# Optimization experiments

Measured on AMD Instinct MI355X. Metric: run time of the kernel, lower is better.

## Reference

```python
import jax, jax.numpy as jnp
import numpy as np

BETA = 0.9
NORM_EPS = 1e-12  # torch F.normalize default eps


def _sqdist(u, v):
    # ||u||^2 + ||v||^2 - 2 u v^T  (matches module's dist())
    return (u ** 2).sum(1, keepdims=True) + (v ** 2).sum(1) - 2.0 * u @ v.T


def setup_inputs() -> dict:
    key = jax.random.key(0)
    k1, k2 = jax.random.split(key)
    z = jax.random.normal(k1, (16, 4096, 128), dtype=jnp.float32)
    # codebook: unit-norm rows (Hypersphere.random_uniform init)
    w = jax.random.normal(k2, (1024, 128), dtype=jnp.float32)
    emb_w = w / jnp.linalg.norm(w, axis=1, keepdims=True)
    return {"z": z, "emb_w": emb_w}


def reference(z, emb_w):
    B, N, D = z.shape
    n_e = emb_w.shape[0]
    zf = z.reshape(-1, D)  # [B*N, D]

    # codebook self-distances + stats
    cd = _sqdist(emb_w, emb_w)                      # [n_e, n_e]
    min_distance = jnp.sort(cd, axis=0)[1]          # kthvalue(cd, 2, dim=0)
    mean_cb_distance = min_distance.mean()
    mean_cb_variance = jnp.var(cd, axis=1, ddof=1).mean()  # torch.var unbiased

    # quantisation: argmin over codebook
    d = _sqdist(zf, emb_w)                          # [B*N, n_e]
    idx = jnp.argmin(d, axis=1)                     # [B*N]
    z_q = emb_w[idx].reshape(z.shape)               # [B, N, D]

    # F.normalize default dim=1 applied to the 3D tensor -> normalize over N axis
    zn = z_q / jnp.maximum(jnp.linalg.norm(z_q, axis=1, keepdims=True), NORM_EPS)

    sg = jax.lax.stop_gradient
    # legacy loss
    loss = jnp.mean((sg(z_q) - z) ** 2) + BETA * jnp.mean((z_q - sg(z)) ** 2)

    # straight-through estimator
    z_q_st = z + sg(z_q - z)

    # sampled_idx buffer of length B*n_e, scatter 1s at the encoding indices
    sampled_idx = jnp.zeros(B * n_e, dtype=z.dtype).at[idx].set(1.0).reshape(B, n_e)

    si = idx.reshape(B, N)
    return (z_q_st, loss, sampled_idx, idx.reshape(B, -1),
            mean_cb_variance, mean_cb_distance, si, zn)
```

## Files before the change

kernel.cpp:

```cpp
#include <hip/hip_runtime.h>
#include <math.h>

#define D       128
#define NE      1024
#define NROWS   65536
#define NB      16

#define OUT_ZQ    0
#define OUT_LOSS  8388608
#define OUT_SAMP  8388609
#define OUT_IDX   8404993
#define OUT_VAR   8470529
#define OUT_DIST  8470530
#define OUT_SI    8470531
#define OUT_ZN    8536067

#define SCR       8536068
#define SCR_WL    (SCR + 65536)
#define SCR_CNT   (SCR + 131072)
#define SCR_LIST  (SCR + 131073)

#define WS_IDX    0
#define WS_WW     65536
#define WS_FLAGS  66560
#define WS_MIN2   67584
#define WS_VAR    68608
#define WS_LOSSP  69632
#define WS_COLSQP 70144
#define WS_COLSQ  135680

#define MARGIN 2e-3f

typedef __attribute__((ext_vector_type(8))) short s16x8;
typedef __attribute__((ext_vector_type(4))) float f32x4;

#define GLDS16(gp, lp)                                                        \
  __builtin_amdgcn_global_load_lds(                                           \
      (const __attribute__((address_space(1))) unsigned int*)(gp),            \
      (__attribute__((address_space(3))) unsigned int*)(lp), 16, 0, 0)

__device__ __forceinline__ unsigned short f2bf(float f) {
  unsigned int u = __float_as_uint(f);
  return (unsigned short)((u + 0x7FFFu + ((u >> 16) & 1u)) >> 16);
}
__device__ __forceinline__ float bf2f(unsigned short h) {
  return __uint_as_float(((unsigned int)h) << 16);
}

__device__ __forceinline__ float npsq_sum128(const float* p) {
  float a[8];
#pragma unroll
  for (int m = 0; m < 8; ++m) a[m] = __fmul_rn(p[m], p[m]);
  for (int k = 8; k < 128; k += 8) {
#pragma unroll
    for (int m = 0; m < 8; ++m) a[m] = __fadd_rn(a[m], __fmul_rn(p[k + m], p[k + m]));
  }
  float s01 = __fadd_rn(a[0], a[1]);
  float s23 = __fadd_rn(a[2], a[3]);
  float s45 = __fadd_rn(a[4], a[5]);
  float s67 = __fadd_rn(a[6], a[7]);
  return __fadd_rn(__fadd_rn(s01, s23), __fadd_rn(s45, s67));
}

__global__ __launch_bounds__(256) void k_wsplit(const float* __restrict__ w,
                                                float* __restrict__ out,
                                                float* __restrict__ ws) {
  int u = blockIdx.x * 256 + threadIdx.x;
  int c = u >> 4, j = u & 15;
  const float4* p = (const float4*)(w + c * D + j * 8);
  float4 f0 = p[0], f1 = p[1];
  float ff[8] = {f0.x, f0.y, f0.z, f0.w, f1.x, f1.y, f1.z, f1.w};
  s16x8 h, l;
#pragma unroll
  for (int e = 0; e < 8; ++e) {
    unsigned short hb = f2bf(ff[e]);
    h[e] = (short)hb;
    l[e] = (short)f2bf(ff[e] - bf2f(hb));
  }
  unsigned int by = ((unsigned int)(c * 256 + j * 16)) ^ ((unsigned int)((c & 15) << 4));
  *(s16x8*)((char*)(out + SCR) + by)    = h;
  *(s16x8*)((char*)(out + SCR_WL) + by) = l;
  if (u < NE) {
    ws[WS_WW + u] = npsq_sum128(w + u * D);
    ((int*)ws)[WS_FLAGS + u] = 0;
  }
  if (u == 0) ((int*)out)[SCR_CNT] = 0;
}

__global__ __launch_bounds__(256) void k_cb(const float* __restrict__ w,
                                            float* __restrict__ wsf,
                                            float* __restrict__ out) {
  __shared__ unsigned short Lw[2][16384];
  __shared__ float Lww[1024];
  const int t    = threadIdx.x;
  const int lane = t & 63;
  const int wq   = t >> 6;
  const int n    = lane & 15;
  const int q    = lane >> 4;
  const int i0   = blockIdx.x * 64 + wq * 16;

  const unsigned short* whg = (const unsigned short*)(out + SCR);
  const unsigned short* wlg = (const unsigned short*)(out + SCR_WL);

#define CSTAGE(BUF, P) do {                                              \
    const unsigned short* _wh = whg + (size_t)(P) * 8192;                \
    const unsigned short* _wl = wlg + (size_t)(P) * 8192;                \
    _Pragma("unroll")                                                    \
    for (int _it = 0; _it < 4; ++_it) {                                  \
      int _ci = _it * 256 + t;                                           \
      GLDS16(_wh + _ci * 8, &Lw[BUF][_ci * 8]);                          \
      GLDS16(_wl + _ci * 8, &Lw[BUF][8192 + _ci * 8]);                   \
    } } while (0)

  CSTAGE(0, 0);
  for (int i = t; i < 1024; i += 256) Lww[i] = wsf[WS_WW + i];

  s16x8 AH[4], AL[4];
  {
    const float* wr = w + (size_t)(i0 + n) * D;
#pragma unroll
    for (int ks = 0; ks < 4; ++ks) {
      float4 f0 = *(const float4*)(wr + ks * 32 + q * 8);
      float4 f1 = *(const float4*)(wr + ks * 32 + q * 8 + 4);
      float ff[8] = {f0.x, f0.y, f0.z, f0.w, f1.x, f1.y, f1.z, f1.w};
      s16x8 h, l;
#pragma unroll
      for (int j = 0; j < 8; ++j) {
        unsigned short hb = f2bf(ff[j]);
        h[j] = (short)hb;
        l[j] = (short)f2bf(ff[j] - bf2f(hb));
      }
      AH[ks] = h; AL[ks] = l;
    }
  }
  float wwi[4];
#pragma unroll
  for (int r = 0; r < 4; ++r) wwi[r] = wsf[WS_WW + i0 + q * 4 + r];

  float m1[4], m2[4], S[4], Q[4];
#pragma unroll
  for (int r = 0; r < 4; ++r) { m1[r] = INFINITY; m2[r] = INFINITY; S[r] = 0.f; Q[r] = 0.f; }

  __syncthreads();

  for (int p = 0; p < 16; ++p) {
    const int buf = p & 1;
    if (p < 15) CSTAGE(buf ^ 1, p + 1);

    for (int ct = 0; ct < 4; ++ct) {
      const int cL = ct * 16 + n;
      const int c  = p * 64 + cL;
      const float wwj = Lww[c];
      f32x4 aX = (f32x4){0.f, 0.f, 0.f, 0.f};
      f32x4 aY = (f32x4){0.f, 0.f, 0.f, 0.f};
#pragma unroll
      for (int ks = 0; ks < 4; ++ks) {
        unsigned int off = (unsigned int)(cL * 256) +
                           (((unsigned int)(64 * ks + 16 * q)) ^ ((unsigned int)(cL & 15) << 4));
        s16x8 BH = *(const s16x8*)((const char*)&Lw[buf][0] + off);
        s16x8 BL = *(const s16x8*)((const char*)&Lw[buf][8192] + off);
        aX = __builtin_amdgcn_mfma_f32_16x16x32_bf16(AH[ks], BH, aX, 0, 0, 0);
        aY = __builtin_amdgcn_mfma_f32_16x16x32_bf16(AH[ks], BL, aY, 0, 0, 0);
        aY = __builtin_amdgcn_mfma_f32_16x16x32_bf16(AL[ks], BH, aY, 0, 0, 0);
      }
#pragma unroll
      for (int r = 0; r < 4; ++r) {
        float dot = aX[r] + aY[r];
        float d = __fsub_rn(__fadd_rn(wwi[r], wwj), __fmul_rn(2.f, dot));
        if (d < m1[r]) { m2[r] = m1[r]; m1[r] = d; } else m2[r] = fminf(m2[r], d);
        S[r] += d; Q[r] = fmaf(d, d, Q[r]);
      }
    }
    __syncthreads();
  }

#pragma unroll
  for (int r = 0; r < 4; ++r) {
    float a1 = m1[r], a2 = m2[r], s = S[r], qq = Q[r];
#pragma unroll
    for (int mask = 1; mask < 16; mask <<= 1) {
      float b1 = __shfl_xor(a1, mask, 64);
      float b2 = __shfl_xor(a2, mask, 64);
      float bs = __shfl_xor(s,  mask, 64);
      float bq = __shfl_xor(qq, mask, 64);
      a2 = fminf(fminf(a2, b2), fmaxf(a1, b1));
      a1 = fminf(a1, b1);
      s += bs; qq += bq;
    }
    if (n == 0) {
      int row = i0 + q * 4 + r;
      wsf[WS_MIN2 + row] = a2;
      wsf[WS_VAR + row] = (qq - s * s / (float)NE) / (float)(NE - 1);
    }
  }
#undef CSTAGE
}

__global__ __launch_bounds__(512, 2) void k_qmfma(const float* __restrict__ z,
                                                  float* __restrict__ wsf,
                                                  float* __restrict__ out) {
  __shared__ unsigned short Lw[2][16384];
  __shared__ float Lww[1024];
  const int t    = threadIdx.x;
  const int lane = t & 63;
  const int wq   = t >> 6;
  const int n    = lane & 15;
  const int q    = lane >> 4;
  const int rowb = blockIdx.x * 256 + wq * 32;

  const unsigned short* whg = (const unsigned short*)(out + SCR);
  const unsigned short* wlg = (const unsigned short*)(out + SCR_WL);

#define QSTAGE(BUF, P) do {                                              \
    const unsigned short* _wh = whg + (size_t)(P) * 8192;                \
    const unsigned short* _wl = wlg + (size_t)(P) * 8192;                \
    _Pragma("unroll")                                                    \
    for (int _it = 0; _it < 2; ++_it) {                                  \
      int _ci = _it * 512 + t;                                           \
      GLDS16(_wh + _ci * 8, &Lw[BUF][_ci * 8]);                          \
      GLDS16(_wl + _ci * 8, &Lw[BUF][8192 + _ci * 8]);                   \
    } } while (0)

  QSTAGE(0, 0);
  for (int i = t; i < 1024; i += 512) Lww[i] = wsf[WS_WW + i];

  s16x8 AH[2][4], AL[2][4];
#pragma unroll
  for (int rt = 0; rt < 2; ++rt) {
    const float* zr = z + (size_t)(rowb + rt * 16 + n) * D;
#pragma unroll
    for (int ks = 0; ks < 4; ++ks) {
      float4 f0 = *(const float4*)(zr + ks * 32 + q * 8);
      float4 f1 = *(const float4*)(zr + ks * 32 + q * 8 + 4);
      float ff[8] = {f0.x, f0.y, f0.z, f0.w, f1.x, f1.y, f1.z, f1.w};
      s16x8 h, l;
#pragma unroll
      for (int j = 0; j < 8; ++j) {
        unsigned short hb = f2bf(ff[j]);
        h[j] = (short)hb;
        l[j] = (short)f2bf(ff[j] - bf2f(hb));
      }
      AH[rt][ks] = h; AL[rt][ks] = l;
    }
  }

  float m1[2][4], m2[2][4]; int i1[2][4];
#pragma unroll
  for (int rt = 0; rt < 2; ++rt)
#pragma unroll
    for (int r = 0; r < 4; ++r) { m1[rt][r] = INFINITY; m2[rt][r] = INFINITY; i1[rt][r] = 0; }

  __syncthreads();

  for (int p = 0; p < 16; ++p) {
    const int buf = p & 1;
    if (p < 15) QSTAGE(buf ^ 1, p + 1);

    for (int ct = 0; ct < 4; ++ct) {
      const int cL = ct * 16 + n;
      const int c  = p * 64 + cL;
      const float wwc = Lww[c];
      f32x4 aX[2], aY[2];
#pragma unroll
      for (int rt = 0; rt < 2; ++rt) {
        aX[rt] = (f32x4){0.f, 0.f, 0.f, 0.f};
        aY[rt] = (f32x4){0.f, 0.f, 0.f, 0.f};
      }
#pragma unroll
      for (int ks = 0; ks < 4; ++ks) {
        unsigned int off = (unsigned int)(cL * 256) +
                           (((unsigned int)(64 * ks + 16 * q)) ^ ((unsigned int)(cL & 15) << 4));
        s16x8 BH = *(const s16x8*)((const char*)&Lw[buf][0] + off);
        s16x8 BL = *(const s16x8*)((const char*)&Lw[buf][8192] + off);
#pragma unroll
        for (int rt = 0; rt < 2; ++rt) {
          aX[rt] = __builtin_amdgcn_mfma_f32_16x16x32_bf16(AH[rt][ks], BH, aX[rt], 0, 0, 0);
          aY[rt] = __builtin_amdgcn_mfma_f32_16x16x32_bf16(AH[rt][ks], BL, aY[rt], 0, 0, 0);
          aY[rt] = __builtin_amdgcn_mfma_f32_16x16x32_bf16(AL[rt][ks], BH, aY[rt], 0, 0, 0);
        }
      }
#pragma unroll
      for (int rt = 0; rt < 2; ++rt)
#pragma unroll
        for (int r = 0; r < 4; ++r) {
          float v = fmaf(-2.f, aX[rt][r] + aY[rt][r], wwc);
          if (v < m1[rt][r]) { m2[rt][r] = m1[rt][r]; m1[rt][r] = v; i1[rt][r] = c; }
          else m2[rt][r] = fminf(m2[rt][r], v);
        }
    }
    __syncthreads();
  }

#pragma unroll
  for (int rt = 0; rt < 2; ++rt)
#pragma unroll
    for (int r = 0; r < 4; ++r) {
      float a1 = m1[rt][r], a2 = m2[rt][r]; int ai = i1[rt][r];
#pragma unroll
      for (int mask = 1; mask < 16; mask <<= 1) {
        float b1 = __shfl_xor(a1, mask, 64);
        float b2 = __shfl_xor(a2, mask, 64);
        int   bi = __shfl_xor(ai, mask, 64);
        a2 = fminf(fminf(a2, b2), fmaxf(a1, b1));
        bool take = (b1 < a1) || (b1 == a1 && bi < ai);
        a1 = take ? b1 : a1; ai = take ? bi : ai;
      }
      if (n == 0) {
        int grow = rowb + rt * 16 + q * 4 + r;
        if (a2 - a1 > MARGIN) {
          ((int*)wsf)[WS_IDX + grow] = ai;
          out[OUT_IDX + grow] = (float)ai;
          out[OUT_SI  + grow] = (float)ai;
          ((int*)wsf)[WS_FLAGS + ai] = 1;
        } else {
          int pos = atomicAdd(((int*)out) + SCR_CNT, 1);
          ((int*)out)[SCR_LIST + pos] = grow;
        }
      }
    }
#undef QSTAGE
}

__global__ __launch_bounds__(256) void k_fallback(const float* __restrict__ z,
                                                  const float* __restrict__ w,
                                                  float* __restrict__ wsf,
                                                  float* __restrict__ out) {
  const int t = threadIdx.x;
  const int count = ((const int*)out)[SCR_CNT];
  const int* list = ((const int*)out) + SCR_LIST;
  __shared__ float zrow[128];
  __shared__ float zzs;
  __shared__ float rv[256];
  __shared__ int   ri[256];
  for (int i = blockIdx.x; i < count; i += gridDim.x) {
    int row = list[i];
    __syncthreads();
    if (t < 32) ((float4*)zrow)[t] = ((const float4*)(z + (size_t)row * D))[t];
    __syncthreads();
    if (t < 8) {
      float a = __fmul_rn(zrow[t], zrow[t]);
#pragma unroll
      for (int k = 8; k < 128; k += 8)
        a = __fadd_rn(a, __fmul_rn(zrow[k + t], zrow[k + t]));
      float s1 = __fadd_rn(a,  __shfl_xor(a, 1, 64));
      float s2 = __fadd_rn(s1, __shfl_xor(s1, 2, 64));
      float s3 = __fadd_rn(s2, __shfl_xor(s2, 4, 64));
      if (t == 0) zzs = s3;
    }
    __syncthreads();
    float zz = zzs;
    float bv = INFINITY; int bi = 0;
    const float4* z4 = (const float4*)zrow;
    for (int cc = 0; cc < 4; ++cc) {
      int c = cc * 256 + t;
      const float4* wp = (const float4*)(w + (size_t)c * D);
      float acc = 0.f;
#pragma unroll
      for (int k4 = 0; k4 < 32; ++k4) {
        float4 a = wp[k4];
        float4 zv = z4[k4];
        acc = fmaf(zv.x, a.x, acc); acc = fmaf(zv.y, a.y, acc);
        acc = fmaf(zv.z, a.z, acc); acc = fmaf(zv.w, a.w, acc);
      }
      float d = __fsub_rn(__fadd_rn(zz, wsf[WS_WW + c]), __fmul_rn(2.f, acc));
      if (d < bv) { bv = d; bi = c; }
    }
    rv[t] = bv; ri[t] = bi;
    __syncthreads();
    for (int s = 128; s > 0; s >>= 1) {
      if (t < s) {
        float v2 = rv[t + s]; int i2 = ri[t + s];
        if (v2 < rv[t] || (v2 == rv[t] && i2 < ri[t])) { rv[t] = v2; ri[t] = i2; }
      }
      __syncthreads();
    }
    if (t == 0) {
      int mi = ri[0];
      ((int*)wsf)[WS_IDX + row] = mi;
      out[OUT_IDX + row] = (float)mi;
      out[OUT_SI  + row] = (float)mi;
      ((int*)wsf)[WS_FLAGS + mi] = 1;
    }
  }
}

__global__ __launch_bounds__(256) void k_gather(const float* __restrict__ z,
                                                const float* __restrict__ w,
                                                float* __restrict__ ws,
                                                float* __restrict__ out) {
  __shared__ float csp[32][8][4];
  __shared__ float lred[256];
  const int t = threadIdx.x, blk = blockIdx.x;
  const int c4 = t & 31, rg = t >> 5;
  float lp = 0.f;
  float csx = 0.f, csy = 0.f, csz = 0.f, csw = 0.f;
  for (int m = 0; m < 16; ++m) {
    int r  = rg + 8 * m;
    int gr = blk * 128 + r;
    int idx = ((const int*)ws)[WS_IDX + gr];
    float4 qv = *(const float4*)&w[idx * D + c4 * 4];
    float4 zv = *(const float4*)&z[(size_t)gr * D + c4 * 4];
    *(float4*)&out[OUT_ZQ + (size_t)gr * D + c4 * 4] = qv;
    float dx = qv.x - zv.x, dy = qv.y - zv.y, dz = qv.z - zv.z, dw = qv.w - zv.w;
    lp = fmaf(dx, dx, lp); lp = fmaf(dy, dy, lp);
    lp = fmaf(dz, dz, lp); lp = fmaf(dw, dw, lp);
    csx = fmaf(qv.x, qv.x, csx); csy = fmaf(qv.y, qv.y, csy);
    csz = fmaf(qv.z, qv.z, csz); csw = fmaf(qv.w, qv.w, csw);
  }
  csp[c4][rg][0] = csx; csp[c4][rg][1] = csy;
  csp[c4][rg][2] = csz; csp[c4][rg][3] = csw;
  lred[t] = lp;
  __syncthreads();
  for (int s = 128; s > 0; s >>= 1) {
    if (t < s) lred[t] += lred[t + s];
    __syncthreads();
  }
  if (t == 0) ws[WS_LOSSP + blk] = lred[0];
  if (t < 128) {
    int dcol = t;
    float s = 0.f;
    for (int g = 0; g < 8; ++g) s += csp[dcol >> 2][g][dcol & 3];
    ws[WS_COLSQP + blk * 128 + dcol] = s;
  }
}

__global__ __launch_bounds__(256) void k_zn(const float* __restrict__ ws,
                                            const float* __restrict__ w,
                                            float* __restrict__ out) {
  const int t = threadIdx.x, blk = blockIdx.x;
  const int c4 = t & 31, rg = t >> 5;
  const int b = blk >> 5;
  float csx = 0.f, csy = 0.f, csz = 0.f, csw = 0.f;
  for (int rb = 0; rb < 32; ++rb) {
    float4 pp = *(const float4*)&ws[WS_COLSQP + (size_t)(b * 32 + rb) * 128 + c4 * 4];
    csx += pp.x; csy += pp.y; csz += pp.z; csw += pp.w;
  }
  float nx = fmaxf(sqrtf(csx), 1e-12f);
  float ny = fmaxf(sqrtf(csy), 1e-12f);
  float nz = fmaxf(sqrtf(csz), 1e-12f);
  float nw = fmaxf(sqrtf(csw), 1e-12f);
  for (int m = 0; m < 16; ++m) {
    int gr = blk * 128 + rg + 8 * m;
    int idx = ((const int*)ws)[WS_IDX + gr];
    float4 qv = *(const float4*)&w[idx * D + c4 * 4];
    size_t o = (size_t)gr * D + c4 * 4;
    out[OUT_ZN + o + 0] = qv.x / nx;
    out[OUT_ZN + o + 1] = qv.y / ny;
    out[OUT_ZN + o + 2] = qv.z / nz;
    out[OUT_ZN + o + 3] = qv.w / nw;
  }
  if (blk == 0) {
    __shared__ float f1[256], f2[256], f3[256];
    __syncthreads();
    f1[t] = ws[WS_LOSSP + t] + ws[WS_LOSSP + t + 256];
    f2[t] = (ws[WS_MIN2 + t] + ws[WS_MIN2 + t + 512]) +
            (ws[WS_MIN2 + t + 256] + ws[WS_MIN2 + t + 768]);
    f3[t] = (ws[WS_VAR + t] + ws[WS_VAR + t + 512]) +
            (ws[WS_VAR + t + 256] + ws[WS_VAR + t + 768]);
    __syncthreads();
    for (int s = 128; s > 0; s >>= 1) {
      if (t < s) { f1[t] += f1[t + s]; f2[t] += f2[t + s]; f3[t] += f3[t + s]; }
      __syncthreads();
    }
    if (t == 0) {
      float m = f1[0] / 8388608.f;
      out[OUT_LOSS] = m + 0.9f * m;
      out[OUT_VAR]  = f3[0] / 1024.f;
      out[OUT_DIST] = f2[0] / 1024.f;
    }
    const int* flags = (const int*)ws + WS_FLAGS;
    for (int i = t; i < NB * NE; i += 256)
      out[OUT_SAMP + i] = (i < NE && flags[i] != 0) ? 1.f : 0.f;
  }
}

extern "C" void kernel_launch(void* const* d_in, const int* in_sizes, int n_in,
                              void* d_out, int out_size, void* d_ws, size_t ws_size,
                              hipStream_t stream) {
  const float* z = (const float*)d_in[0];
  const float* w = (const float*)d_in[1];
  float* out = (float*)d_out;
  float* ws  = (float*)d_ws;

  hipLaunchKernelGGL(k_wsplit,   dim3(64),   dim3(256), 0, stream, w, out, ws);
  hipLaunchKernelGGL(k_cb,       dim3(16),   dim3(256), 0, stream, w, ws, out);
  hipLaunchKernelGGL(k_qmfma,    dim3(256),  dim3(512), 0, stream, z, ws, out);
  hipLaunchKernelGGL(k_fallback, dim3(1024), dim3(256), 0, stream, z, w, ws, out);
  hipLaunchKernelGGL(k_gather,   dim3(512),  dim3(256), 0, stream, z, w, ws, out);
  hipLaunchKernelGGL(k_zn,       dim3(512),  dim3(256), 0, stream, ws, w, out);
}
```

Before: 134.7 us.

## Split codebook self-distance kernel across more blocks with per-wave column ranges

The codebook statistics kernel now runs 64 blocks, each handling 16 codebook rows. Each of its four waves covers a quarter of the columns, reading the bf16 split codebook straight from global memory instead of double-buffering it through LDS. Per-wave min/second-min/sum/sum-of-squares partials are merged through shared memory at the end. This aims to raise parallelism in a small 16-block kernel that sits serially before the main quantisation kernel, at the cost of more redundant global/L2 reads of the codebook and an extra cross-wave reduction.

```diff
diff --git a/kernel.cpp b/kernel.cpp
--- a/kernel.cpp
+++ b/kernel.cpp
@@ -90,30 +90,16 @@
 __global__ __launch_bounds__(256) void k_cb(const float* __restrict__ w,
                                             float* __restrict__ wsf,
                                             float* __restrict__ out) {
-  __shared__ unsigned short Lw[2][16384];
-  __shared__ float Lww[1024];
+  __shared__ float cm1[4][16], cm2[4][16], cS[4][16], cQ[4][16];
   const int t    = threadIdx.x;
   const int lane = t & 63;
   const int wq   = t >> 6;
   const int n    = lane & 15;
   const int q    = lane >> 4;
-  const int i0   = blockIdx.x * 64 + wq * 16;
-
-  const unsigned short* whg = (const unsigned short*)(out + SCR);
-  const unsigned short* wlg = (const unsigned short*)(out + SCR_WL);
-
-#define CSTAGE(BUF, P) do {                                              \
-    const unsigned short* _wh = whg + (size_t)(P) * 8192;                \
-    const unsigned short* _wl = wlg + (size_t)(P) * 8192;                \
-    _Pragma("unroll")                                                    \
-    for (int _it = 0; _it < 4; ++_it) {                                  \
-      int _ci = _it * 256 + t;                                           \
-      GLDS16(_wh + _ci * 8, &Lw[BUF][_ci * 8]);                          \
-      GLDS16(_wl + _ci * 8, &Lw[BUF][8192 + _ci * 8]);                   \
-    } } while (0)
-
-  CSTAGE(0, 0);
-  for (int i = t; i < 1024; i += 256) Lww[i] = wsf[WS_WW + i];
+  const int i0   = blockIdx.x * 16;
+
+  const char* whg = (const char*)(out + SCR);
+  const char* wlg = (const char*)(out + SCR_WL);
 
   s16x8 AH[4], AL[4];
   {
@@ -141,37 +127,28 @@
 #pragma unroll
   for (int r = 0; r < 4; ++r) { m1[r] = INFINITY; m2[r] = INFINITY; S[r] = 0.f; Q[r] = 0.f; }
 
-  __syncthreads();
-
-  for (int p = 0; p < 16; ++p) {
-    const int buf = p & 1;
-    if (p < 15) CSTAGE(buf ^ 1, p + 1);
-
-    for (int ct = 0; ct < 4; ++ct) {
-      const int cL = ct * 16 + n;
-      const int c  = p * 64 + cL;
-      const float wwj = Lww[c];
-      f32x4 aX = (f32x4){0.f, 0.f, 0.f, 0.f};
-      f32x4 aY = (f32x4){0.f, 0.f, 0.f, 0.f};
-#pragma unroll
-      for (int ks = 0; ks < 4; ++ks) {
-        unsigned int off = (unsigned int)(cL * 256) +
-                           (((unsigned int)(64 * ks + 16 * q)) ^ ((unsigned int)(cL & 15) << 4));
-        s16x8 BH = *(const s16x8*)((const char*)&Lw[buf][0] + off);
-        s16x8 BL = *(const s16x8*)((const char*)&Lw[buf][8192] + off);
-        aX = __builtin_amdgcn_mfma_f32_16x16x32_bf16(AH[ks], BH, aX, 0, 0, 0);
-        aY = __builtin_amdgcn_mfma_f32_16x16x32_bf16(AH[ks], BL, aY, 0, 0, 0);
-        aY = __builtin_amdgcn_mfma_f32_16x16x32_bf16(AL[ks], BH, aY, 0, 0, 0);
-      }
-#pragma unroll
-      for (int r = 0; r < 4; ++r) {
-        float dot = aX[r] + aY[r];
-        float d = __fsub_rn(__fadd_rn(wwi[r], wwj), __fmul_rn(2.f, dot));
-        if (d < m1[r]) { m2[r] = m1[r]; m1[r] = d; } else m2[r] = fminf(m2[r], d);
-        S[r] += d; Q[r] = fmaf(d, d, Q[r]);
-      }
-    }
-    __syncthreads();
+  for (int ct = 0; ct < 16; ++ct) {
+    const int c = wq * 256 + ct * 16 + n;
+    const float wwj = wsf[WS_WW + c];
+    f32x4 aX = (f32x4){0.f, 0.f, 0.f, 0.f};
+    f32x4 aY = (f32x4){0.f, 0.f, 0.f, 0.f};
+#pragma unroll
+    for (int ks = 0; ks < 4; ++ks) {
+      unsigned int off = (unsigned int)(c * 256) +
+                         (((unsigned int)(64 * ks + 16 * q)) ^ ((unsigned int)((c & 15) << 4)));
+      s16x8 BH = *(const s16x8*)(whg + off);
+      s16x8 BL = *(const s16x8*)(wlg + off);
+      aX = __builtin_amdgcn_mfma_f32_16x16x32_bf16(AH[ks], BH, aX, 0, 0, 0);
+      aY = __builtin_amdgcn_mfma_f32_16x16x32_bf16(AH[ks], BL, aY, 0, 0, 0);
+      aY = __builtin_amdgcn_mfma_f32_16x16x32_bf16(AL[ks], BH, aY, 0, 0, 0);
+    }
+#pragma unroll
+    for (int r = 0; r < 4; ++r) {
+      float dot = aX[r] + aY[r];
+      float d = __fsub_rn(__fadd_rn(wwi[r], wwj), __fmul_rn(2.f, dot));
+      if (d < m1[r]) { m2[r] = m1[r]; m1[r] = d; } else m2[r] = fminf(m2[r], d);
+      S[r] += d; Q[r] = fmaf(d, d, Q[r]);
+    }
   }
 
 #pragma unroll
@@ -188,12 +165,23 @@
       s += bs; qq += bq;
     }
     if (n == 0) {
-      int row = i0 + q * 4 + r;
-      wsf[WS_MIN2 + row] = a2;
-      wsf[WS_VAR + row] = (qq - s * s / (float)NE) / (float)(NE - 1);
-    }
-  }
-#undef CSTAGE
+      int rl = q * 4 + r;
+      cm1[wq][rl] = a1; cm2[wq][rl] = a2; cS[wq][rl] = s; cQ[wq][rl] = qq;
+    }
+  }
+  __syncthreads();
+  if (t < 16) {
+    float a1 = cm1[0][t], a2 = cm2[0][t], s = cS[0][t], qq = cQ[0][t];
+#pragma unroll
+    for (int v = 1; v < 4; ++v) {
+      float b1 = cm1[v][t], b2 = cm2[v][t];
+      a2 = fminf(fminf(a2, b2), fmaxf(a1, b1));
+      a1 = fminf(a1, b1);
+      s += cS[v][t]; qq += cQ[v][t];
+    }
+    wsf[WS_MIN2 + i0 + t] = a2;
+    wsf[WS_VAR + i0 + t] = (qq - s * s / (float)NE) / (float)(NE - 1);
+  }
 }
 
 __global__ __launch_bounds__(512, 2) void k_qmfma(const float* __restrict__ z,
@@ -483,7 +471,7 @@
   float* ws  = (float*)d_ws;
 
   hipLaunchKernelGGL(k_wsplit,   dim3(64),   dim3(256), 0, stream, w, out, ws);
-  hipLaunchKernelGGL(k_cb,       dim3(16),   dim3(256), 0, stream, w, ws, out);
+  hipLaunchKernelGGL(k_cb,       dim3(64),   dim3(256), 0, stream, w, ws, out);
   hipLaunchKernelGGL(k_qmfma,    dim3(256),  dim3(512), 0, stream, z, ws, out);
   hipLaunchKernelGGL(k_fallback, dim3(1024), dim3(256), 0, stream, z, w, ws, out);
   hipLaunchKernelGGL(k_gather,   dim3(512),  dim3(256), 0, stream, z, w, ws, out);
```

Result: slower. 140.5 us (+4.3%).
